# Kernel tuning notes

Hardware: AMD Instinct MI355X
Metric: run time of the kernel (lower is better)

The kernel has to match this reference:

```python
import jax, jax.numpy as jnp
import numpy as np

B, S, E, H = 4, 1024, 1024, 16

def setup_inputs() -> dict:
    key = jax.random.key(0)
    ks = jax.random.split(key, 7)
    sc = 0.02
    return {
        "queries": jax.random.normal(ks[0], (B, S, E), jnp.float32),
        "keys": jax.random.normal(ks[1], (B, S, E), jnp.float32),
        "values": jax.random.normal(ks[2], (B, S, E), jnp.float32),
        "Wq_w": jax.random.normal(ks[3], (E, E), jnp.float32) * sc,
        "Wq_b": jax.random.normal(ks[4], (E,), jnp.float32) * sc,
        "Wo_w": jax.random.normal(ks[5], (E, E), jnp.float32) * sc,
        "Wo_b": jax.random.normal(ks[6], (E,), jnp.float32) * sc,
        "num_heads": H,
    }

def reference(queries, keys, values, Wq_w, Wq_b, Wo_w, Wo_b, num_heads):
    b, s, e = queries.shape
    dh = e // num_heads

    def proj_heads(x):
        # NOTE: original module applies Wq to q, k AND v (bug kept faithfully)
        y = x @ Wq_w.T + Wq_b                      # [b, s, e]
        return y.reshape(b, s, num_heads, dh)      # [b, s, h, dh]

    q = proj_heads(queries)
    k = proj_heads(keys)
    v = proj_heads(values)

    scores = jnp.einsum('bqhd,bkhd->bhqk', q, k) / jnp.sqrt(jnp.asarray(dh, q.dtype))
    attn = jax.nn.softmax(scores, axis=-1)         # [b, h, q, k]
    out = jnp.einsum('bhqk,bkhd->bqhd', attn, v)   # [b, s, h, dh]
    out = out.reshape(b, s, e)
    return out @ Wo_w.T + Wo_b
```

## Files before the change

### kernel.cpp

```cpp
#include <hip/hip_runtime.h>
#include <stdint.h>


typedef __attribute__((ext_vector_type(8))) short bf16x8;
typedef __attribute__((ext_vector_type(4))) float f32x4;
typedef __attribute__((ext_vector_type(4))) short short4v;

#define GLOAD_LDS(gp, lp)                                                      \
  __builtin_amdgcn_global_load_lds(                                            \
      (__attribute__((address_space(1))) void*)(gp),                           \
      (__attribute__((address_space(3))) void*)(lp), 16, 0, 0)

__device__ __forceinline__ unsigned short f2bf(float f) {
  union { float f; unsigned u; } v; v.f = f;
  unsigned r = v.u + 0x7FFFu + ((v.u >> 16) & 1u);
  return (unsigned short)(r >> 16);
}

__global__ void cvt_all(const float* __restrict__ q, const float* __restrict__ k,
                        const float* __restrict__ v, const float* __restrict__ wq,
                        const float* __restrict__ wo, short* __restrict__ dst) {
  int i = blockIdx.x * 256 + threadIdx.x;
  const float* src; int j;
  if (i < 1048576)      { src = q;  j = i; }
  else if (i < 2097152) { src = k;  j = i - 1048576; }
  else if (i < 3145728) { src = v;  j = i - 2097152; }
  else if (i < 3407872) { src = wq; j = i - 3145728; }
  else                  { src = wo; j = i - 3407872; }
  float4 f = reinterpret_cast<const float4*>(src)[j];
  short4v o;
  o.x = (short)f2bf(f.x); o.y = (short)f2bf(f.y);
  o.z = (short)f2bf(f.z); o.w = (short)f2bf(f.w);
  reinterpret_cast<short4v*>(dst)[i] = o;
}

template<int EPI>
__global__ __launch_bounds__(256, 2)
void gemm_bt(const short* __restrict__ A, const short* __restrict__ Bw,
             const float* __restrict__ bias,
             short* __restrict__ qkv, float* __restrict__ outf)
{
  __shared__ short As[128 * 64];
  __shared__ short Bs[128 * 64];
  const int tid  = threadIdx.x;
  const int lane = tid & 63;
  const int g    = lane >> 4;
  const int r7   = lane & 7;
  const int w    = tid >> 6;
  const int wm   = w >> 1, wn = w & 1;

  const int orig = blockIdx.y * 8 + blockIdx.x;
  const int cpx  = (gridDim.x * gridDim.y) >> 3;
  const int t    = (orig & 7) * cpx + (orig >> 3);
  const int m0   = (t >> 3) * 128, n0 = (t & 7) * 128;

  f32x4 acc[4][4] = {};

  for (int k0 = 0; k0 < 1024; k0 += 64) {
#pragma unroll
    for (int c = 0; c < 4; c++) {
      int L   = c * 256 + tid;
      int row = L >> 3;
      int col = ((L & 7) ^ (row & 7)) * 8;
      GLOAD_LDS(A  + (m0 + row) * 1024 + k0 + col, As + L * 8);
      GLOAD_LDS(Bw + (n0 + row) * 1024 + k0 + col, Bs + L * 8);
    }
    __syncthreads();
#pragma unroll
    for (int kk = 0; kk < 2; kk++) {
      bf16x8 av[4], bv[4];
#pragma unroll
      for (int mi = 0; mi < 4; mi++) {
        int row = wm * 64 + mi * 16 + (lane & 15);
        av[mi] = *(const bf16x8*)&As[row * 64 + (((kk * 4 + g) ^ r7) * 8)];
      }
#pragma unroll
      for (int ni = 0; ni < 4; ni++) {
        int row = wn * 64 + ni * 16 + (lane & 15);
        bv[ni] = *(const bf16x8*)&Bs[row * 64 + (((kk * 4 + g) ^ r7) * 8)];
      }
#pragma unroll
      for (int mi = 0; mi < 4; mi++)
#pragma unroll
        for (int ni = 0; ni < 4; ni++)
          acc[mi][ni] = __builtin_amdgcn_mfma_f32_16x16x32_bf16(av[mi], bv[ni], acc[mi][ni], 0, 0, 0);
    }
    __syncthreads();
  }

  if (EPI == 0) {
    const int inp = m0 >> 12;
#pragma unroll
    for (int mi = 0; mi < 4; mi++) {
#pragma unroll
      for (int ni = 0; ni < 4; ni++) {
        const int coll = n0 + wn * 64 + ni * 16 + (lane & 15);
        const float bv = bias[coll];
        const int rbase = m0 + wm * 64 + mi * 16 + (lane >> 4) * 4;
        const int hh = coll >> 6, d = coll & 63;
        if (inp < 2) {
#pragma unroll
          for (int j = 0; j < 4; j++) {
            int rowl = rbase + j;
            int bb = (rowl >> 10) & 3, s = rowl & 1023;
            qkv[(((inp * 4 + bb) * 16 + hh) * 1024 + s) * 64 + d] =
                (short)f2bf(acc[mi][ni][j] + bv);
          }
        } else {
          int bb = (rbase >> 10) & 3, s0 = rbase & 1023;
          short4v o;
          o.x = (short)f2bf(acc[mi][ni][0] + bv);
          o.y = (short)f2bf(acc[mi][ni][1] + bv);
          o.z = (short)f2bf(acc[mi][ni][2] + bv);
          o.w = (short)f2bf(acc[mi][ni][3] + bv);
          *(short4v*)&qkv[8 * 1024 * 1024 + ((bb * 16 + hh) * 64 + d) * 1024 + s0] = o;
        }
      }
    }
  } else {
#pragma unroll
    for (int mi = 0; mi < 4; mi++) {
#pragma unroll
      for (int ni = 0; ni < 4; ni++) {
        const int coll = n0 + wn * 64 + ni * 16 + (lane & 15);
        const float bv = bias[coll];
        const int rbase = m0 + wm * 64 + mi * 16 + (lane >> 4) * 4;
#pragma unroll
        for (int j = 0; j < 4; j++)
          outf[(rbase + j) * 1024 + coll] = acc[mi][ni][j] + bv;
      }
    }
  }
}

__global__ __launch_bounds__(256, 2)
void attn_kernel(const short* __restrict__ qkv, short* __restrict__ O)
{
  __shared__ short Ks[2][64 * 64];
  __shared__ short VTs[2][64 * 64];
  __shared__ short QPs[64 * 64];

  const int tid  = threadIdx.x;
  const int lane = tid & 63;
  const int g    = lane >> 4, r7 = lane & 7;
  const int w    = tid >> 6;

  const int t   = (blockIdx.x & 7) * 128 + (blockIdx.x >> 3);
  const int qt  = t & 15, hh = (t >> 4) & 15, bb = t >> 8;
  const int q0  = qt * 64;

  const short* Qg = qkv + (bb * 16 + hh) * 1024 * 64;
  const short* Kg = qkv + 4 * 1024 * 1024 + (bb * 16 + hh) * 1024 * 64;
  const short* Vg = qkv + 8 * 1024 * 1024 + (bb * 16 + hh) * 64 * 1024;

#pragma unroll
  for (int c = 0; c < 2; c++) {
    int L = c * 256 + tid;
    int row = L >> 3;
    int col = ((L & 7) ^ (row & 7)) * 8;
    GLOAD_LDS(Qg + (q0 + row) * 64 + col, QPs + L * 8);
    GLOAD_LDS(Kg + row * 64 + col,        &Ks[0][L * 8]);
    GLOAD_LDS(Vg + row * 1024 + col,      &VTs[0][L * 8]);
  }
  __syncthreads();
  bf16x8 qf[2];
  {
    const int qrow = w * 16 + (lane & 15);
    qf[0] = *(const bf16x8*)&QPs[qrow * 64 + ((g ^ r7) * 8)];
    qf[1] = *(const bf16x8*)&QPs[qrow * 64 + (((4 + g) ^ r7) * 8)];
  }

  const float SC = 0.125f * 1.44269504f;
  float m_run[4], l_run[4];
  f32x4 acc_o[4] = {};
#pragma unroll
  for (int j = 0; j < 4; j++) { m_run[j] = -1e30f; l_run[j] = 0.0f; }

  int cur = 0;
  for (int kt = 0; kt < 16; kt++) {
    if (kt < 15) {
#pragma unroll
      for (int c = 0; c < 2; c++) {
        int L = c * 256 + tid;
        int row = L >> 3;
        int col = ((L & 7) ^ (row & 7)) * 8;
        GLOAD_LDS(Kg + ((kt + 1) * 64 + row) * 64 + col, &Ks[cur ^ 1][L * 8]);
        GLOAD_LDS(Vg + row * 1024 + (kt + 1) * 64 + col, &VTs[cur ^ 1][L * 8]);
      }
    }

    f32x4 sa[4] = {};
#pragma unroll
    for (int kk = 0; kk < 2; kk++) {
#pragma unroll
      for (int ni = 0; ni < 4; ni++) {
        int krow = ni * 16 + (lane & 15);
        bf16x8 kf = *(const bf16x8*)&Ks[cur][krow * 64 + (((kk * 4 + g) ^ r7) * 8)];
        sa[ni] = __builtin_amdgcn_mfma_f32_16x16x32_bf16(qf[kk], kf, sa[ni], 0, 0, 0);
      }
    }
    float mt[4];
#pragma unroll
    for (int j = 0; j < 4; j++)
      mt[j] = fmaxf(fmaxf(sa[0][j], sa[1][j]), fmaxf(sa[2][j], sa[3][j]));
#pragma unroll
    for (int off = 1; off < 16; off <<= 1)
#pragma unroll
      for (int j = 0; j < 4; j++)
        mt[j] = fmaxf(mt[j], __shfl_xor(mt[j], off));
    float alpha[4], rs[4];
#pragma unroll
    for (int j = 0; j < 4; j++) {
      float mn = fmaxf(m_run[j], mt[j] * SC);
      alpha[j] = __builtin_amdgcn_exp2f(m_run[j] - mn);
      m_run[j] = mn;
      rs[j] = 0.0f;
    }
#pragma unroll
    for (int ni = 0; ni < 4; ni++) {
      int col = ni * 16 + (lane & 15);
#pragma unroll
      for (int j = 0; j < 4; j++) {
        int row = w * 16 + g * 4 + j;
        float p = __builtin_amdgcn_exp2f(sa[ni][j] * SC - m_run[j]);
        rs[j] += p;
        QPs[row * 64 + (col ^ ((row & 7) << 3))] = (short)f2bf(p);
      }
    }
#pragma unroll
    for (int off = 1; off < 16; off <<= 1)
#pragma unroll
      for (int j = 0; j < 4; j++)
        rs[j] += __shfl_xor(rs[j], off);
#pragma unroll
    for (int j = 0; j < 4; j++)
      l_run[j] = l_run[j] * alpha[j] + rs[j];
#pragma unroll
    for (int di = 0; di < 4; di++)
#pragma unroll
      for (int j = 0; j < 4; j++)
        acc_o[di][j] *= alpha[j];
#pragma unroll
    for (int kk = 0; kk < 2; kk++) {
      int prow = w * 16 + (lane & 15);
      bf16x8 pf = *(const bf16x8*)&QPs[prow * 64 + (((kk * 4 + g) ^ r7) * 8)];
#pragma unroll
      for (int di = 0; di < 4; di++) {
        int vrow = di * 16 + (lane & 15);
        bf16x8 vf = *(const bf16x8*)&VTs[cur][vrow * 64 + (((kk * 4 + g) ^ r7) * 8)];
        acc_o[di] = __builtin_amdgcn_mfma_f32_16x16x32_bf16(pf, vf, acc_o[di], 0, 0, 0);
      }
    }
    __syncthreads();
    cur ^= 1;
  }

#pragma unroll
  for (int di = 0; di < 4; di++) {
    int d = hh * 64 + di * 16 + (lane & 15);
#pragma unroll
    for (int j = 0; j < 4; j++) {
      int q = q0 + w * 16 + g * 4 + j;
      O[(bb * 1024 + q) * 1024 + d] = (short)f2bf(acc_o[di][j] / l_run[j]);
    }
  }
}

extern "C" void kernel_launch(void* const* d_in, const int* in_sizes, int n_in,
                              void* d_out, int out_size, void* d_ws, size_t ws_size,
                              hipStream_t stream)
{
  (void)in_sizes; (void)n_in; (void)out_size; (void)ws_size;
  const float* q    = (const float*)d_in[0];
  const float* k    = (const float*)d_in[1];
  const float* v    = (const float*)d_in[2];
  const float* Wq_w = (const float*)d_in[3];
  const float* Wq_b = (const float*)d_in[4];
  const float* Wo_w = (const float*)d_in[5];
  const float* Wo_b = (const float*)d_in[6];
  float* out = (float*)d_out;

  short* ws   = (short*)d_ws;
  short* Xbf  = ws;
  short* Obf  = ws;
  short* Wqb  = ws + 12582912;
  short* Wob  = ws + 13631488;
  short* qkv  = ws + 14680064;

  cvt_all<<<14336, 256, 0, stream>>>(q, k, v, Wq_w, Wo_w, ws);

  dim3 gp(8, 96);
  gemm_bt<0><<<gp, 256, 0, stream>>>(Xbf, Wqb, Wq_b, qkv, nullptr);

  attn_kernel<<<1024, 256, 0, stream>>>(qkv, Obf);

  dim3 gf(8, 32);
  gemm_bt<1><<<gf, 256, 0, stream>>>(Obf, Wob, Wo_b, nullptr, out);
}
```

Before: 209.3 us.

## Transpose attention MFMA operands, lazy rescale softmax, packed P stores

Swaps the MFMA operand order so each lane holds one query row's scores. This cuts the row max/sum reductions from four-step shuffles over four rows to two shuffles on a scalar. Adds a conditional online-softmax rescale that only fires when the max grows by more than a threshold. P is written to LDS with packed bf16 conversion and vector stores, and the output is stored as short4 vectors. Also raises the launch bound to 4 waves/SIMD and adds s_setprio around MFMA blocks, which risks register pressure and numerical drift from the deferred rescale.

```diff
diff --git a/kernel.cpp b/kernel.cpp
--- a/kernel.cpp
+++ b/kernel.cpp
@@ -15,6 +15,11 @@
   union { float f; unsigned u; } v; v.f = f;
   unsigned r = v.u + 0x7FFFu + ((v.u >> 16) & 1u);
   return (unsigned short)(r >> 16);
+}
+__device__ __forceinline__ unsigned cvt_pk_bf16(float lo, float hi) {
+  unsigned r;
+  asm("v_cvt_pk_bf16_f32 %0, %1, %2" : "=v"(r) : "v"(lo), "v"(hi));
+  return r;
 }
 
 __global__ void cvt_all(const float* __restrict__ q, const float* __restrict__ k,
@@ -133,15 +138,16 @@
   }
 }
 
-__global__ __launch_bounds__(256, 2)
+__global__ __launch_bounds__(256, 4)
 void attn_kernel(const short* __restrict__ qkv, short* __restrict__ O)
 {
-  __shared__ short Ks[2][64 * 64];
-  __shared__ short VTs[2][64 * 64];
-  __shared__ short QPs[64 * 64];
+  __shared__ __align__(16) short Qs[64 * 64];
+  __shared__ __align__(16) short Ks[2][64 * 64];
+  __shared__ __align__(16) short VTs[2][64 * 64];
 
   const int tid  = threadIdx.x;
   const int lane = tid & 63;
+  const int l15  = lane & 15;
   const int g    = lane >> 4, r7 = lane & 7;
   const int w    = tid >> 6;
 
@@ -158,23 +164,25 @@
     int L = c * 256 + tid;
     int row = L >> 3;
     int col = ((L & 7) ^ (row & 7)) * 8;
-    GLOAD_LDS(Qg + (q0 + row) * 64 + col, QPs + L * 8);
+    GLOAD_LDS(Qg + (q0 + row) * 64 + col, Qs + L * 8);
     GLOAD_LDS(Kg + row * 64 + col,        &Ks[0][L * 8]);
     GLOAD_LDS(Vg + row * 1024 + col,      &VTs[0][L * 8]);
   }
   __syncthreads();
   bf16x8 qf[2];
   {
-    const int qrow = w * 16 + (lane & 15);
-    qf[0] = *(const bf16x8*)&QPs[qrow * 64 + ((g ^ r7) * 8)];
-    qf[1] = *(const bf16x8*)&QPs[qrow * 64 + (((4 + g) ^ r7) * 8)];
-  }
+    const int qrow = w * 16 + l15;
+    qf[0] = *(const bf16x8*)&Qs[qrow * 64 + ((g ^ r7) * 8)];
+    qf[1] = *(const bf16x8*)&Qs[qrow * 64 + (((4 + g) ^ r7) * 8)];
+  }
+  __syncthreads();
+
+  unsigned* PT = reinterpret_cast<unsigned*>(Qs) + w * 512;
+  const int X = (l15 & 7) << 2;
 
   const float SC = 0.125f * 1.44269504f;
-  float m_run[4], l_run[4];
+  float m_run = -1e30f, l_run = 0.0f;
   f32x4 acc_o[4] = {};
-#pragma unroll
-  for (int j = 0; j < 4; j++) { m_run[j] = -1e30f; l_run[j] = 0.0f; }
 
   int cur = 0;
   for (int kt = 0; kt < 16; kt++) {
@@ -190,79 +198,81 @@
     }
 
     f32x4 sa[4] = {};
+    __builtin_amdgcn_s_setprio(1);
 #pragma unroll
     for (int kk = 0; kk < 2; kk++) {
 #pragma unroll
       for (int ni = 0; ni < 4; ni++) {
-        int krow = ni * 16 + (lane & 15);
+        int krow = ni * 16 + l15;
         bf16x8 kf = *(const bf16x8*)&Ks[cur][krow * 64 + (((kk * 4 + g) ^ r7) * 8)];
-        sa[ni] = __builtin_amdgcn_mfma_f32_16x16x32_bf16(qf[kk], kf, sa[ni], 0, 0, 0);
-      }
-    }
-    float mt[4];
-#pragma unroll
-    for (int j = 0; j < 4; j++)
-      mt[j] = fmaxf(fmaxf(sa[0][j], sa[1][j]), fmaxf(sa[2][j], sa[3][j]));
-#pragma unroll
-    for (int off = 1; off < 16; off <<= 1)
-#pragma unroll
-      for (int j = 0; j < 4; j++)
-        mt[j] = fmaxf(mt[j], __shfl_xor(mt[j], off));
-    float alpha[4], rs[4];
-#pragma unroll
-    for (int j = 0; j < 4; j++) {
-      float mn = fmaxf(m_run[j], mt[j] * SC);
-      alpha[j] = __builtin_amdgcn_exp2f(m_run[j] - mn);
-      m_run[j] = mn;
-      rs[j] = 0.0f;
-    }
+        sa[ni] = __builtin_amdgcn_mfma_f32_16x16x32_bf16(kf, qf[kk], sa[ni], 0, 0, 0);
+      }
+    }
+    __builtin_amdgcn_s_setprio(0);
+
+    float mt;
+    {
+      float a = fmaxf(fmaxf(sa[0][0], sa[0][1]), fmaxf(sa[0][2], sa[0][3]));
+      float b = fmaxf(fmaxf(sa[1][0], sa[1][1]), fmaxf(sa[1][2], sa[1][3]));
+      float c = fmaxf(fmaxf(sa[2][0], sa[2][1]), fmaxf(sa[2][2], sa[2][3]));
+      float d = fmaxf(fmaxf(sa[3][0], sa[3][1]), fmaxf(sa[3][2], sa[3][3]));
+      mt = fmaxf(fmaxf(a, b), fmaxf(c, d)) * SC;
+    }
+    if (__any(mt - m_run > 8.0f)) {
+      float x = fmaxf(mt, __shfl_xor(mt, 16));
+      x = fmaxf(x, __shfl_xor(x, 32));
+      float mn = fmaxf(m_run, x);
+      float alpha = __builtin_amdgcn_exp2f(m_run - mn);
+      m_run = mn;
+      l_run *= alpha;
+#pragma unroll
+      for (int di = 0; di < 4; di++)
+#pragma unroll
+        for (int j = 0; j < 4; j++) acc_o[di][j] *= alpha;
+    }
+    float ts = 0.0f;
 #pragma unroll
     for (int ni = 0; ni < 4; ni++) {
-      int col = ni * 16 + (lane & 15);
-#pragma unroll
-      for (int j = 0; j < 4; j++) {
-        int row = w * 16 + g * 4 + j;
-        float p = __builtin_amdgcn_exp2f(sa[ni][j] * SC - m_run[j]);
-        rs[j] += p;
-        QPs[row * 64 + (col ^ ((row & 7) << 3))] = (short)f2bf(p);
-      }
-    }
-#pragma unroll
-    for (int off = 1; off < 16; off <<= 1)
-#pragma unroll
-      for (int j = 0; j < 4; j++)
-        rs[j] += __shfl_xor(rs[j], off);
-#pragma unroll
-    for (int j = 0; j < 4; j++)
-      l_run[j] = l_run[j] * alpha[j] + rs[j];
-#pragma unroll
-    for (int di = 0; di < 4; di++)
-#pragma unroll
-      for (int j = 0; j < 4; j++)
-        acc_o[di][j] *= alpha[j];
+      float p0 = __builtin_amdgcn_exp2f(sa[ni][0] * SC - m_run);
+      float p1 = __builtin_amdgcn_exp2f(sa[ni][1] * SC - m_run);
+      float p2 = __builtin_amdgcn_exp2f(sa[ni][2] * SC - m_run);
+      float p3 = __builtin_amdgcn_exp2f(sa[ni][3] * SC - m_run);
+      ts += (p0 + p1) + (p2 + p3);
+      unsigned u0 = cvt_pk_bf16(p0, p1);
+      unsigned u1 = cvt_pk_bf16(p2, p3);
+      uint2 uu; uu.x = u0; uu.y = u1;
+      *reinterpret_cast<uint2*>(&PT[l15 * 32 + ((8 * ni + 2 * g) ^ X)]) = uu;
+    }
+    ts += __shfl_xor(ts, 16);
+    ts += __shfl_xor(ts, 32);
+    l_run += ts;
+
+    __builtin_amdgcn_s_setprio(1);
 #pragma unroll
     for (int kk = 0; kk < 2; kk++) {
-      int prow = w * 16 + (lane & 15);
-      bf16x8 pf = *(const bf16x8*)&QPs[prow * 64 + (((kk * 4 + g) ^ r7) * 8)];
+      bf16x8 pB = *reinterpret_cast<const bf16x8*>(&PT[l15 * 32 + ((16 * kk + 4 * g) ^ X)]);
 #pragma unroll
       for (int di = 0; di < 4; di++) {
-        int vrow = di * 16 + (lane & 15);
+        int vrow = di * 16 + l15;
         bf16x8 vf = *(const bf16x8*)&VTs[cur][vrow * 64 + (((kk * 4 + g) ^ r7) * 8)];
-        acc_o[di] = __builtin_amdgcn_mfma_f32_16x16x32_bf16(pf, vf, acc_o[di], 0, 0, 0);
-      }
-    }
+        acc_o[di] = __builtin_amdgcn_mfma_f32_16x16x32_bf16(vf, pB, acc_o[di], 0, 0, 0);
+      }
+    }
+    __builtin_amdgcn_s_setprio(0);
     __syncthreads();
     cur ^= 1;
   }
 
+  const float linv = 1.0f / l_run;
+  const int q = q0 + w * 16 + l15;
 #pragma unroll
   for (int di = 0; di < 4; di++) {
-    int d = hh * 64 + di * 16 + (lane & 15);
-#pragma unroll
-    for (int j = 0; j < 4; j++) {
-      int q = q0 + w * 16 + g * 4 + j;
-      O[(bb * 1024 + q) * 1024 + d] = (short)f2bf(acc_o[di][j] / l_run[j]);
-    }
+    short4v o;
+    o.x = (short)f2bf(acc_o[di][0] * linv);
+    o.y = (short)f2bf(acc_o[di][1] * linv);
+    o.z = (short)f2bf(acc_o[di][2] * linv);
+    o.w = (short)f2bf(acc_o[di][3] * linv);
+    *(short4v*)&O[(bb * 1024 + q) * 1024 + hh * 64 + di * 16 + g * 4] = o;
   }
 }
 
```

New measurement: 189.4 us. -9.5%, faster.
